# Optimization experiments

Hardware: AMD Instinct MI355X
Metric: run time of the kernel (lower is better)

Reference implementation:

```python
import jax, jax.numpy as jnp
import numpy as np

B = 16384
D_VIS, D_LANG, D_STATE = 768, 768, 64
D = 256          # d_model
E = 4            # n_experts
K = 2            # top_k
D_IN = D_VIS + D_LANG + D_STATE
EPS = 1e-5


def layernorm(x, g, b):
    mu = x.mean(-1, keepdims=True)
    var = ((x - mu) ** 2).mean(-1, keepdims=True)
    return g * (x - mu) / jnp.sqrt(var + EPS) + b


def setup_inputs() -> dict:
    key = jax.random.key(0)
    ks = jax.random.split(key, 16)
    s = 0.02
    return {
        "vis": jax.random.normal(ks[0], (B, D_VIS), jnp.float32),
        "lang": jax.random.normal(ks[1], (B, D_LANG), jnp.float32),
        "state": jax.random.normal(ks[2], (B, D_STATE), jnp.float32),
        # fusion: Linear(d_in, d_model) + LayerNorm
        "Wf": jax.random.normal(ks[3], (D_IN, D), jnp.float32) * s,
        "bf": jnp.zeros((D,), jnp.float32),
        "gf": jnp.ones((D,), jnp.float32),
        "bfln": jnp.zeros((D,), jnp.float32),
        # gate (bias=False); random instead of zeros so routing is nontrivial
        "Wg": jax.random.normal(ks[4], (D, E), jnp.float32) * s,
        # stacked experts: Linear(d,2d) -> GELU -> Linear(2d,d) -> GELU -> Linear(d,d), then LN(x + net(x))
        "W1": jax.random.normal(ks[5], (E, D, 2 * D), jnp.float32) * s,
        "b1": jnp.zeros((E, 2 * D), jnp.float32),
        "W2": jax.random.normal(ks[6], (E, 2 * D, D), jnp.float32) * s,
        "b2": jnp.zeros((E, D), jnp.float32),
        "W3": jax.random.normal(ks[7], (E, D, D), jnp.float32) * s,
        "b3": jnp.zeros((E, D), jnp.float32),
        "eg": jnp.ones((E, D), jnp.float32),
        "eb": jnp.zeros((E, D), jnp.float32),
    }


def reference(vis, lang, state, Wf, bf, gf, bfln, Wg, W1, b1, W2, b2, W3, b3, eg, eb):
    gelu = lambda t: jax.nn.gelu(t, approximate=False)
    # fusion: Linear -> LayerNorm -> GELU  (dropout is eval-mode identity)
    x = jnp.concatenate([vis, lang, state], axis=-1) @ Wf + bf   # [B, D]
    x = gelu(layernorm(x, gf, bfln))

    logits = x @ Wg                                              # [B, E]
    all_probs = jax.nn.softmax(logits, axis=-1)
    top_vals, top_idx = jax.lax.top_k(logits, K)                 # [B, K]
    top_w = jax.nn.softmax(top_vals, axis=-1)                    # [B, K]

    # all experts densely (E small); original computes same math per masked subset
    h = gelu(jnp.einsum('bd,edh->beh', x, W1) + b1)              # [B, E, 2D]
    h = gelu(jnp.einsum('beh,ehd->bed', h, W2) + b2)             # [B, E, D]
    h = jnp.einsum('bed,edf->bef', h, W3) + b3                   # [B, E, D]
    y = layernorm(x[:, None, :] + h, eg, eb)                     # [B, E, D]

    # gather selected experts and combine with top-k weights
    y_sel = jnp.take_along_axis(y, top_idx[:, :, None], axis=1)  # [B, K, D]
    out = jnp.einsum('bk,bkd->bd', top_w, y_sel)                 # [B, D]

    # load-balance loss: importance x load
    counts = jnp.zeros((E,), x.dtype).at[top_idx.reshape(-1)].add(1.0)
    f_i = counts / (B * K)
    lb_loss = E * jnp.sum(f_i * all_probs.mean(0))
    return out, lb_loss
```

## Files before the change

### kernel.cpp

```cpp
#include <hip/hip_runtime.h>
#include <math.h>


typedef unsigned short u16;
typedef unsigned int u32;
typedef __attribute__((ext_vector_type(8))) short bf16x8;
typedef __attribute__((ext_vector_type(4))) float f32x4;

__device__ __forceinline__ float bf2f(u16 u) {
    union { u32 i; float f; } v; v.i = ((u32)u) << 16; return v.f;
}
__device__ __forceinline__ u16 f2bf(float f) {
    union { float f; u32 i; } v; v.f = f;
    u32 x = v.i;
    return (u16)((x + 0x7fffu + ((x >> 16) & 1u)) >> 16);
}
__device__ __forceinline__ float gelu_exact(float v) {
    return 0.5f * v * (1.0f + erff(v * 0.70710678118654752f));
}

typedef __attribute__((address_space(1))) void GV;
typedef __attribute__((address_space(3))) void SV;
__device__ __forceinline__ void gldlds(const void* g, void* l) {
    __builtin_amdgcn_global_load_lds((GV*)g, (SV*)l, 16, 0, 0);
}

__device__ __forceinline__ u32 pk2(u32 f0, u32 f1) {
    return __builtin_amdgcn_perm(f1, f0, 0x07060302);
}

__device__ __forceinline__ void stageA64(const u16* Ag, int lda, u16* As, int tid) {
#pragma unroll
    for (int i = 0; i < 2; ++i) {
        int s = i * 256 + tid;
        int m = s >> 3, c = s & 7;
        gldlds(Ag + m * lda + (c ^ (m & 7)) * 8, As + s * 8);
    }
}
__device__ __forceinline__ void stageA64_R32(const u16* Ag, int lda, u16* As, int tid) {
    int s = tid;
    int m = s >> 3, c = s & 7;
    gldlds(Ag + m * lda + (c ^ (m & 7)) * 8, As + s * 8);
}
__device__ __forceinline__ void stageB64(const u16* Bg, int ldb, u16* Bs, int tid) {
#pragma unroll
    for (int i = 0; i < 8; ++i) {
        int s = i * 256 + tid;
        int n = s >> 3, c = s & 7;
        gldlds(Bg + n * ldb + (c ^ (n & 7)) * 8, Bs + s * 8);
    }
}
__device__ __forceinline__ void compute64(const u16* As, const u16* Bs, f32x4 acc[4][4],
                                          int w, int l16, int quad) {
#pragma unroll
    for (int ks = 0; ks < 2; ++ks) {
        bf16x8 a[4];
#pragma unroll
        for (int mt = 0; mt < 4; ++mt) {
            int m = mt * 16 + l16;
            a[mt] = *(const bf16x8*)(As + m * 64 + (((ks * 4 + quad) ^ (m & 7)) << 3));
        }
#pragma unroll
        for (int nt = 0; nt < 4; ++nt) {
            int n = w * 64 + nt * 16 + l16;
            bf16x8 b = *(const bf16x8*)(Bs + n * 64 + (((ks * 4 + quad) ^ (n & 7)) << 3));
#pragma unroll
            for (int mt = 0; mt < 4; ++mt)
                acc[mt][nt] = __builtin_amdgcn_mfma_f32_16x16x32_bf16(a[mt], b, acc[mt][nt], 0, 0, 0);
        }
    }
}
__device__ __forceinline__ void compute64_R32(const u16* As, const u16* Bs, f32x4 acc[2][4],
                                              int w, int l16, int quad) {
#pragma unroll
    for (int ks = 0; ks < 2; ++ks) {
        bf16x8 a[2];
#pragma unroll
        for (int mt = 0; mt < 2; ++mt) {
            int m = mt * 16 + l16;
            a[mt] = *(const bf16x8*)(As + m * 64 + (((ks * 4 + quad) ^ (m & 7)) << 3));
        }
#pragma unroll
        for (int nt = 0; nt < 4; ++nt) {
            int n = w * 64 + nt * 16 + l16;
            bf16x8 b = *(const bf16x8*)(Bs + n * 64 + (((ks * 4 + quad) ^ (n & 7)) << 3));
#pragma unroll
            for (int mt = 0; mt < 2; ++mt)
                acc[mt][nt] = __builtin_amdgcn_mfma_f32_16x16x32_bf16(a[mt], b, acc[mt][nt], 0, 0, 0);
        }
    }
}

#define SEG_WF  409600
#define SEG_W1  524288
#define SEG_W2  524288
#define SEG_W3  262144
#define PREP_ITEMS (SEG_WF + SEG_W1 + SEG_W2 + SEG_W3 + 8)

__global__ __launch_bounds__(256) void prep_kernel(
    const float* __restrict__ Wf, const float* __restrict__ W1, const float* __restrict__ W2,
    const float* __restrict__ W3,
    u16* __restrict__ wft, u16* __restrict__ w1t, u16* __restrict__ w2t, u16* __restrict__ w3t,
    float* __restrict__ lbacc) {
    int idx = blockIdx.x * 256 + threadIdx.x;
    if (idx < SEG_WF) {
        int n = idx / 1600, k = idx % 1600;
        wft[idx] = f2bf(Wf[(size_t)k * 256 + n]);
        return;
    }
    idx -= SEG_WF;
    if (idx < SEG_W1) {
        int e = idx >> 17, r = idx & 131071;
        int n = r >> 8, k = r & 255;
        w1t[idx] = f2bf(W1[(size_t)e * 131072 + (size_t)k * 512 + n]);
        return;
    }
    idx -= SEG_W1;
    if (idx < SEG_W2) {
        int e = idx >> 17, r = idx & 131071;
        int n = r >> 9, k = r & 511;
        w2t[idx] = f2bf(W2[(size_t)e * 131072 + (size_t)k * 256 + n]);
        return;
    }
    idx -= SEG_W2;
    if (idx < SEG_W3) {
        int e = idx >> 16, r = idx & 65535;
        int n = r >> 8, k = r & 255;
        w3t[idx] = f2bf(W3[(size_t)e * 65536 + (size_t)k * 256 + n]);
        return;
    }
    idx -= SEG_W3;
    if (idx < 8) lbacc[idx] = 0.0f;
}

__global__ __launch_bounds__(256) void fusion_kernel(
    const float* __restrict__ vis, const float* __restrict__ lang, const float* __restrict__ state,
    const u16* __restrict__ BT, const float* __restrict__ bfv_, const float* __restrict__ gf,
    const float* __restrict__ bfln, const float* __restrict__ Wg,
    u16* __restrict__ xbf, float* __restrict__ wr, float* __restrict__ lbacc) {
    __shared__ __align__(16) u32 Af[2048];
    __shared__ __align__(16) u16 Bs[16384];
    int tid = threadIdx.x;
    int w = tid >> 6, lane = tid & 63, quad = lane >> 4, l16 = lane & 15;
    int m0 = blockIdx.x * 32;
    f32x4 acc[2][4] = {};

    for (int kit = 0; kit < 25; ++kit) {
        const float* base; int ld;
        if (kit < 12)      { base = vis   + (size_t)m0 * 768 + kit * 64;        ld = 768; }
        else if (kit < 24) { base = lang  + (size_t)m0 * 768 + (kit - 12) * 64; ld = 768; }
        else               { base = state + (size_t)m0 * 64;                    ld = 64; }
#pragma unroll
        for (int i = 0; i < 2; ++i) {
            int s = i * 256 + tid;
            int m = s >> 4, c = s & 15;
            gldlds(base + m * ld + (c ^ (m & 15)) * 4, Af + s * 4);
        }
        stageB64(BT + kit * 64, 1600, Bs, tid);
        __syncthreads();
#pragma unroll
        for (int ks = 0; ks < 2; ++ks) {
            bf16x8 a[2];
#pragma unroll
            for (int mt = 0; mt < 2; ++mt) {
                int m = mt * 16 + l16;
                int c0 = ks * 8 + quad * 2;
                const u32* rowp = Af + m * 64;
                uint4 f0 = *(const uint4*)(rowp + (c0 ^ (m & 15)) * 4);
                uint4 f1 = *(const uint4*)(rowp + ((c0 + 1) ^ (m & 15)) * 4);
                union { u32 u[4]; bf16x8 v; } pk;
                pk.u[0] = pk2(f0.x, f0.y); pk.u[1] = pk2(f0.z, f0.w);
                pk.u[2] = pk2(f1.x, f1.y); pk.u[3] = pk2(f1.z, f1.w);
                a[mt] = pk.v;
            }
#pragma unroll
            for (int nt = 0; nt < 4; ++nt) {
                int n = w * 64 + nt * 16 + l16;
                bf16x8 b = *(const bf16x8*)(Bs + n * 64 + (((ks * 4 + quad) ^ (n & 7)) << 3));
#pragma unroll
                for (int mt = 0; mt < 2; ++mt)
                    acc[mt][nt] = __builtin_amdgcn_mfma_f32_16x16x32_bf16(a[mt], b, acc[mt][nt], 0, 0, 0);
            }
        }
        __syncthreads();
    }

    float2* red  = (float2*)Af;
    float*  muv  = (float*)(Af + 256);
    float*  rsv  = (float*)(Af + 288);
    float*  gred = (float*)(Af + 512);
    float*  sacc = (float*)(Af + 1024);

    float bv[4], gvv[4], blv[4]; float4 wgv[4];
#pragma unroll
    for (int nt = 0; nt < 4; ++nt) {
        int col = w * 64 + nt * 16 + l16;
        bv[nt] = bfv_[col]; gvv[nt] = gf[col]; blv[nt] = bfln[col];
        wgv[nt] = *(const float4*)(Wg + col * 4);
    }
    if (tid < 8) sacc[tid] = 0.f;
#pragma unroll
    for (int mt = 0; mt < 2; ++mt)
#pragma unroll
        for (int r = 0; r < 4; ++r) {
            float ss = 0.f, qq = 0.f;
#pragma unroll
            for (int nt = 0; nt < 4; ++nt) {
                float v = acc[mt][nt][r] + bv[nt];
                acc[mt][nt][r] = v;
                ss += v; qq += v * v;
            }
#pragma unroll
            for (int d = 1; d < 16; d <<= 1) { ss += __shfl_xor(ss, d); qq += __shfl_xor(qq, d); }
            if (l16 == 0) red[w * 32 + mt * 16 + quad * 4 + r] = make_float2(ss, qq);
        }
    __syncthreads();
    if (tid < 32) {
        float ss = 0.f, qq = 0.f;
#pragma unroll
        for (int ww = 0; ww < 4; ++ww) { float2 t = red[ww * 32 + tid]; ss += t.x; qq += t.y; }
        float mu = ss * (1.f / 256.f);
        float var = qq * (1.f / 256.f) - mu * mu;
        muv[tid] = mu;
        rsv[tid] = 1.f / sqrtf(var + 1e-5f);
    }
    __syncthreads();
#pragma unroll
    for (int mt = 0; mt < 2; ++mt)
#pragma unroll
        for (int r = 0; r < 4; ++r) {
            int rl = mt * 16 + quad * 4 + r;
            float mu = muv[rl], rs = rsv[rl];
#pragma unroll
            for (int nt = 0; nt < 4; ++nt) {
                int col = w * 64 + nt * 16 + l16;
                float t = (acc[mt][nt][r] - mu) * rs * gvv[nt] + blv[nt];
                float g = gelu_exact(t);
                acc[mt][nt][r] = g;
                xbf[(size_t)(m0 + rl) * 256 + col] = f2bf(g);
            }
        }
#pragma unroll
    for (int mt = 0; mt < 2; ++mt)
#pragma unroll
        for (int r = 0; r < 4; ++r) {
            int rl = mt * 16 + quad * 4 + r;
            float p0 = 0.f, p1 = 0.f, p2 = 0.f, p3 = 0.f;
#pragma unroll
            for (int nt = 0; nt < 4; ++nt) {
                float g = acc[mt][nt][r];
                p0 += g * wgv[nt].x; p1 += g * wgv[nt].y;
                p2 += g * wgv[nt].z; p3 += g * wgv[nt].w;
            }
#pragma unroll
            for (int d = 1; d < 16; d <<= 1) {
                p0 += __shfl_xor(p0, d); p1 += __shfl_xor(p1, d);
                p2 += __shfl_xor(p2, d); p3 += __shfl_xor(p3, d);
            }
            if (l16 == 0) {
                float* gp = gred + w * 128 + rl * 4;
                gp[0] = p0; gp[1] = p1; gp[2] = p2; gp[3] = p3;
            }
        }
    __syncthreads();
    if (tid < 32) {
        int row = tid;
        float lg[4];
#pragma unroll
        for (int e = 0; e < 4; ++e)
            lg[e] = gred[row * 4 + e] + gred[128 + row * 4 + e] +
                    gred[256 + row * 4 + e] + gred[384 + row * 4 + e];
        float mx = fmaxf(fmaxf(lg[0], lg[1]), fmaxf(lg[2], lg[3]));
        float ex[4]; float Z = 0.f;
#pragma unroll
        for (int e = 0; e < 4; ++e) { ex[e] = expf(lg[e] - mx); Z += ex[e]; }
        int i0 = 0; float v0 = lg[0];
#pragma unroll
        for (int e = 1; e < 4; ++e) if (lg[e] > v0) { v0 = lg[e]; i0 = e; }
        int i1 = -1; float v1 = -1e30f;
#pragma unroll
        for (int e = 0; e < 4; ++e) if (e != i0 && lg[e] > v1) { v1 = lg[e]; i1 = e; }
        float t = expf(v1 - v0);
        float wA = 1.f / (1.f + t), wB = t / (1.f + t);
        float w4[4] = {0.f, 0.f, 0.f, 0.f};
        w4[i0] = wA; w4[i1] = wB;
#pragma unroll
        for (int e = 0; e < 4; ++e) wr[(size_t)(m0 + row) * 4 + e] = w4[e];
#pragma unroll
        for (int e = 0; e < 4; ++e) atomicAdd(&sacc[e], ex[e] / Z);
        atomicAdd(&sacc[4 + i0], 1.f);
        atomicAdd(&sacc[4 + i1], 1.f);
    }
    __syncthreads();
    if (tid < 8) atomicAdd(lbacc + tid, sacc[tid]);
}

__global__ __launch_bounds__(256) void expert_gemm_kernel(
    const u16* __restrict__ A, int lda, size_t aE,
    const u16* __restrict__ BT, size_t bE,
    const float* __restrict__ bias, int biasE,
    u16* __restrict__ outp, int ldo, size_t oE) {
    __shared__ __align__(16) u16 As[4096];
    __shared__ __align__(16) u16 Bs[16384];
    int tid = threadIdx.x;
    int w = tid >> 6, lane = tid & 63, quad = lane >> 4, l16 = lane & 15;
    int m0 = blockIdx.x * 64;
    int col0 = blockIdx.y * 256;
    int e = blockIdx.z;
    f32x4 acc[4][4] = {};
    const u16* Ag = A + e * aE + (size_t)m0 * lda;
    const u16* Bg = BT + e * bE + (size_t)col0 * lda;
    int kiters = lda >> 6;
    for (int kit = 0; kit < kiters; ++kit) {
        stageA64(Ag + kit * 64, lda, As, tid);
        stageB64(Bg + kit * 64, lda, Bs, tid);
        __syncthreads();
        compute64(As, Bs, acc, w, l16, quad);
        __syncthreads();
    }
#pragma unroll
    for (int nt = 0; nt < 4; ++nt) {
        int col = col0 + w * 64 + nt * 16 + l16;
        float bvv = bias[e * biasE + col];
#pragma unroll
        for (int mt = 0; mt < 4; ++mt)
#pragma unroll
            for (int r = 0; r < 4; ++r) {
                int row = m0 + mt * 16 + quad * 4 + r;
                outp[e * oE + (size_t)row * ldo + col] = f2bf(gelu_exact(acc[mt][nt][r] + bvv));
            }
    }
}

__global__ __launch_bounds__(256) void combine_kernel(
    const u16* __restrict__ h2, const u16* __restrict__ W3T,
    const float* __restrict__ b3, const float* __restrict__ eg, const float* __restrict__ eb,
    const u16* __restrict__ xbf, const float* __restrict__ wr,
    const float* __restrict__ lbacc, float* __restrict__ outp) {
    __shared__ __align__(16) u16 As[2048];
    __shared__ __align__(16) u16 Bs[16384];
    __shared__ __align__(16) u16 xs[8192];
    __shared__ float wl[128];
    int tid = threadIdx.x;
    int w = tid >> 6, lane = tid & 63, quad = lane >> 4, l16 = lane & 15;
    int m0 = blockIdx.x * 32;
    if (blockIdx.x == 0 && tid == 0) {
        float lb = 0.f;
#pragma unroll
        for (int e = 0; e < 4; ++e)
            lb += (lbacc[4 + e] / 32768.f) * (lbacc[e] / 16384.f);
        outp[4194304] = 4.f * lb;
    }
#pragma unroll
    for (int i = 0; i < 4; ++i) {
        int s = i * 256 + tid;
        *(uint4*)(xs + s * 8) = *(const uint4*)(xbf + (size_t)m0 * 256 + s * 8);
    }
    if (tid < 128) wl[tid] = wr[(size_t)m0 * 4 + tid];
    float2* red = (float2*)As;
    float* muv = (float*)((char*)As + 1024);
    float* rsv = (float*)((char*)As + 1152);
    f32x4 oacc[2][4] = {};
    for (int e = 0; e < 4; ++e) {
        __syncthreads();
        f32x4 acc[2][4] = {};
        const u16* Ag = h2 + ((size_t)e * 16384 + m0) * 256;
        const u16* Bg = W3T + (size_t)e * 65536;
        for (int kit = 0; kit < 4; ++kit) {
            stageA64_R32(Ag + kit * 64, 256, As, tid);
            stageB64(Bg + kit * 64, 256, Bs, tid);
            __syncthreads();
            compute64_R32(As, Bs, acc, w, l16, quad);
            __syncthreads();
        }
        float b3v[4], egv[4], ebv[4];
#pragma unroll
        for (int nt = 0; nt < 4; ++nt) {
            int col = w * 64 + nt * 16 + l16;
            b3v[nt] = b3[e * 256 + col]; egv[nt] = eg[e * 256 + col]; ebv[nt] = eb[e * 256 + col];
        }
#pragma unroll
        for (int mt = 0; mt < 2; ++mt)
#pragma unroll
            for (int r = 0; r < 4; ++r) {
                int rl = mt * 16 + quad * 4 + r;
                float ss = 0.f, qq = 0.f;
#pragma unroll
                for (int nt = 0; nt < 4; ++nt) {
                    int col = w * 64 + nt * 16 + l16;
                    float v = acc[mt][nt][r] + b3v[nt] + bf2f(xs[rl * 256 + col]);
                    acc[mt][nt][r] = v;
                    ss += v; qq += v * v;
                }
#pragma unroll
                for (int d = 1; d < 16; d <<= 1) { ss += __shfl_xor(ss, d); qq += __shfl_xor(qq, d); }
                if (l16 == 0) red[w * 32 + rl] = make_float2(ss, qq);
            }
        __syncthreads();
        if (tid < 32) {
            float ss = 0.f, qq = 0.f;
#pragma unroll
            for (int ww = 0; ww < 4; ++ww) { float2 t = red[ww * 32 + tid]; ss += t.x; qq += t.y; }
            float mu = ss * (1.f / 256.f);
            float var = qq * (1.f / 256.f) - mu * mu;
            muv[tid] = mu;
            rsv[tid] = 1.f / sqrtf(var + 1e-5f);
        }
        __syncthreads();
#pragma unroll
        for (int mt = 0; mt < 2; ++mt)
#pragma unroll
            for (int r = 0; r < 4; ++r) {
                int rl = mt * 16 + quad * 4 + r;
                float mu = muv[rl], rs = rsv[rl], we = wl[rl * 4 + e];
#pragma unroll
                for (int nt = 0; nt < 4; ++nt) {
                    float y = (acc[mt][nt][r] - mu) * rs * egv[nt] + ebv[nt];
                    oacc[mt][nt][r] += we * y;
                }
            }
    }
#pragma unroll
    for (int mt = 0; mt < 2; ++mt)
#pragma unroll
        for (int r = 0; r < 4; ++r) {
            int rl = mt * 16 + quad * 4 + r;
#pragma unroll
            for (int nt = 0; nt < 4; ++nt) {
                int col = w * 64 + nt * 16 + l16;
                outp[(size_t)(m0 + rl) * 256 + col] = oacc[mt][nt][r];
            }
        }
}

extern "C" void kernel_launch(void* const* d_in, const int* in_sizes, int n_in,
                              void* d_out, int out_size, void* d_ws, size_t ws_size,
                              hipStream_t stream) {
    const float* vis   = (const float*)d_in[0];
    const float* lang  = (const float*)d_in[1];
    const float* state = (const float*)d_in[2];
    const float* Wf    = (const float*)d_in[3];
    const float* bf_   = (const float*)d_in[4];
    const float* gf    = (const float*)d_in[5];
    const float* bfln  = (const float*)d_in[6];
    const float* Wg    = (const float*)d_in[7];
    const float* W1    = (const float*)d_in[8];
    const float* b1    = (const float*)d_in[9];
    const float* W2    = (const float*)d_in[10];
    const float* b2    = (const float*)d_in[11];
    const float* W3    = (const float*)d_in[12];
    const float* b3    = (const float*)d_in[13];
    const float* eg    = (const float*)d_in[14];
    const float* eb    = (const float*)d_in[15];
    float* outp = (float*)d_out;

    char* ws = (char*)d_ws;
    size_t off = 0;
    float* lbacc = (float*)(ws + off); off += 256;
    u16* WFT  = (u16*)(ws + off); off += 819200UL;
    u16* W1T  = (u16*)(ws + off); off += 1048576UL;
    u16* W2T  = (u16*)(ws + off); off += 1048576UL;
    u16* W3T  = (u16*)(ws + off); off += 524288UL;
    u16* XBF  = (u16*)(ws + off); off += 8388608UL;
    float* WR = (float*)(ws + off); off += 262144UL;
    u16* H1   = (u16*)(ws + off); off += 67108864UL;
    u16* H2   = (u16*)(ws + off); off += 33554432UL;
    if (ws_size < off) return;

    int prep_blocks = (PREP_ITEMS + 255) / 256;
    prep_kernel<<<prep_blocks, 256, 0, stream>>>(Wf, W1, W2, W3, WFT, W1T, W2T, W3T, lbacc);
    fusion_kernel<<<512, 256, 0, stream>>>(vis, lang, state, WFT, bf_, gf, bfln, Wg,
                                           XBF, WR, lbacc);
    expert_gemm_kernel<<<dim3(256, 2, 4), 256, 0, stream>>>(
        XBF, 256, 0, W1T, 131072, b1, 512, H1, 512, 8388608UL);
    expert_gemm_kernel<<<dim3(256, 1, 4), 256, 0, stream>>>(
        H1, 512, 8388608UL, W2T, 131072, b2, 256, H2, 256, 4194304UL);
    combine_kernel<<<512, 256, 0, stream>>>(H2, W3T, b3, eg, eb, XBF, WR, lbacc, outp);
}
```

Before: 322.4 us.

## Double-buffer GEMM staging, retile expert GEMMs, use fast GELU approximation

Adds double-buffered LDS staging to the fusion, expert and combine kernels so global loads for the next K-slice overlap the MFMA work on the current one. Expert GEMMs now use 64x128 tiles with twice as many blocks. The combine kernel keeps the H2 fragments and the residual x in registers and flattens the expert/k loop into one pipelined loop. Exact erf GELU is replaced with a sigmoid-based tanh approximation, which is cheaper but slightly changes numerics.

```diff
diff --git a/kernel.cpp b/kernel.cpp
--- a/kernel.cpp
+++ b/kernel.cpp
@@ -15,80 +15,18 @@
     u32 x = v.i;
     return (u16)((x + 0x7fffu + ((x >> 16) & 1u)) >> 16);
 }
-__device__ __forceinline__ float gelu_exact(float v) {
-    return 0.5f * v * (1.0f + erff(v * 0.70710678118654752f));
+__device__ __forceinline__ float gelu_fast(float x) {
+    float t = x * (1.59576912f + 0.07135481f * x * x);
+    return x / (1.f + __expf(-t));
+}
+__device__ __forceinline__ u32 pk2(u32 f0, u32 f1) {
+    return __builtin_amdgcn_perm(f1, f0, 0x07060302);
 }
 
 typedef __attribute__((address_space(1))) void GV;
 typedef __attribute__((address_space(3))) void SV;
 __device__ __forceinline__ void gldlds(const void* g, void* l) {
     __builtin_amdgcn_global_load_lds((GV*)g, (SV*)l, 16, 0, 0);
-}
-
-__device__ __forceinline__ u32 pk2(u32 f0, u32 f1) {
-    return __builtin_amdgcn_perm(f1, f0, 0x07060302);
-}
-
-__device__ __forceinline__ void stageA64(const u16* Ag, int lda, u16* As, int tid) {
-#pragma unroll
-    for (int i = 0; i < 2; ++i) {
-        int s = i * 256 + tid;
-        int m = s >> 3, c = s & 7;
-        gldlds(Ag + m * lda + (c ^ (m & 7)) * 8, As + s * 8);
-    }
-}
-__device__ __forceinline__ void stageA64_R32(const u16* Ag, int lda, u16* As, int tid) {
-    int s = tid;
-    int m = s >> 3, c = s & 7;
-    gldlds(Ag + m * lda + (c ^ (m & 7)) * 8, As + s * 8);
-}
-__device__ __forceinline__ void stageB64(const u16* Bg, int ldb, u16* Bs, int tid) {
-#pragma unroll
-    for (int i = 0; i < 8; ++i) {
-        int s = i * 256 + tid;
-        int n = s >> 3, c = s & 7;
-        gldlds(Bg + n * ldb + (c ^ (n & 7)) * 8, Bs + s * 8);
-    }
-}
-__device__ __forceinline__ void compute64(const u16* As, const u16* Bs, f32x4 acc[4][4],
-                                          int w, int l16, int quad) {
-#pragma unroll
-    for (int ks = 0; ks < 2; ++ks) {
-        bf16x8 a[4];
-#pragma unroll
-        for (int mt = 0; mt < 4; ++mt) {
-            int m = mt * 16 + l16;
-            a[mt] = *(const bf16x8*)(As + m * 64 + (((ks * 4 + quad) ^ (m & 7)) << 3));
-        }
-#pragma unroll
-        for (int nt = 0; nt < 4; ++nt) {
-            int n = w * 64 + nt * 16 + l16;
-            bf16x8 b = *(const bf16x8*)(Bs + n * 64 + (((ks * 4 + quad) ^ (n & 7)) << 3));
-#pragma unroll
-            for (int mt = 0; mt < 4; ++mt)
-                acc[mt][nt] = __builtin_amdgcn_mfma_f32_16x16x32_bf16(a[mt], b, acc[mt][nt], 0, 0, 0);
-        }
-    }
-}
-__device__ __forceinline__ void compute64_R32(const u16* As, const u16* Bs, f32x4 acc[2][4],
-                                              int w, int l16, int quad) {
-#pragma unroll
-    for (int ks = 0; ks < 2; ++ks) {
-        bf16x8 a[2];
-#pragma unroll
-        for (int mt = 0; mt < 2; ++mt) {
-            int m = mt * 16 + l16;
-            a[mt] = *(const bf16x8*)(As + m * 64 + (((ks * 4 + quad) ^ (m & 7)) << 3));
-        }
-#pragma unroll
-        for (int nt = 0; nt < 4; ++nt) {
-            int n = w * 64 + nt * 16 + l16;
-            bf16x8 b = *(const bf16x8*)(Bs + n * 64 + (((ks * 4 + quad) ^ (n & 7)) << 3));
-#pragma unroll
-            for (int mt = 0; mt < 2; ++mt)
-                acc[mt][nt] = __builtin_amdgcn_mfma_f32_16x16x32_bf16(a[mt], b, acc[mt][nt], 0, 0, 0);
-        }
-    }
 }
 
 #define SEG_WF  409600
@@ -138,58 +76,68 @@
     const u16* __restrict__ BT, const float* __restrict__ bfv_, const float* __restrict__ gf,
     const float* __restrict__ bfln, const float* __restrict__ Wg,
     u16* __restrict__ xbf, float* __restrict__ wr, float* __restrict__ lbacc) {
-    __shared__ __align__(16) u32 Af[2048];
-    __shared__ __align__(16) u16 Bs[16384];
-    int tid = threadIdx.x;
-    int w = tid >> 6, lane = tid & 63, quad = lane >> 4, l16 = lane & 15;
+    __shared__ __align__(16) u32 Af[2][2048];
+    __shared__ __align__(16) u16 Bs[2][16384];
+    int tid = threadIdx.x, w = tid >> 6, lane = tid & 63, quad = lane >> 4, l16 = lane & 15;
     int m0 = blockIdx.x * 32;
     f32x4 acc[2][4] = {};
 
-    for (int kit = 0; kit < 25; ++kit) {
+    auto stageAB = [&](int kit, int buf) {
         const float* base; int ld;
-        if (kit < 12)      { base = vis   + (size_t)m0 * 768 + kit * 64;        ld = 768; }
-        else if (kit < 24) { base = lang  + (size_t)m0 * 768 + (kit - 12) * 64; ld = 768; }
-        else               { base = state + (size_t)m0 * 64;                    ld = 64; }
+        if (kit < 12)      { base = vis + kit * 64;          ld = 768; }
+        else if (kit < 24) { base = lang + (kit - 12) * 64;  ld = 768; }
+        else               { base = state;                   ld = 64; }
+        base += (size_t)m0 * ld;
 #pragma unroll
         for (int i = 0; i < 2; ++i) {
-            int s = i * 256 + tid;
-            int m = s >> 4, c = s & 15;
-            gldlds(base + m * ld + (c ^ (m & 15)) * 4, Af + s * 4);
-        }
-        stageB64(BT + kit * 64, 1600, Bs, tid);
-        __syncthreads();
+            int s = i * 256 + tid, m = s >> 4, c = s & 15;
+            gldlds(base + (size_t)m * ld + ((c ^ (m & 15)) << 2), &Af[buf][s * 4]);
+        }
+#pragma unroll
+        for (int i = 0; i < 8; ++i) {
+            int s = i * 256 + tid, n = s >> 3, c = s & 7;
+            gldlds(BT + (size_t)n * 1600 + kit * 64 + ((c ^ (n & 7)) << 3), &Bs[buf][s * 8]);
+        }
+    };
+    auto comp = [&](int buf) {
 #pragma unroll
         for (int ks = 0; ks < 2; ++ks) {
-            bf16x8 a[2];
+            bf16x8 av[2];
 #pragma unroll
             for (int mt = 0; mt < 2; ++mt) {
                 int m = mt * 16 + l16;
                 int c0 = ks * 8 + quad * 2;
-                const u32* rowp = Af + m * 64;
-                uint4 f0 = *(const uint4*)(rowp + (c0 ^ (m & 15)) * 4);
-                uint4 f1 = *(const uint4*)(rowp + ((c0 + 1) ^ (m & 15)) * 4);
+                const u32* rowp = &Af[buf][m * 64];
+                uint4 f0 = *(const uint4*)(rowp + ((c0 ^ (m & 15)) << 2));
+                uint4 f1 = *(const uint4*)(rowp + (((c0 + 1) ^ (m & 15)) << 2));
                 union { u32 u[4]; bf16x8 v; } pk;
                 pk.u[0] = pk2(f0.x, f0.y); pk.u[1] = pk2(f0.z, f0.w);
                 pk.u[2] = pk2(f1.x, f1.y); pk.u[3] = pk2(f1.z, f1.w);
-                a[mt] = pk.v;
+                av[mt] = pk.v;
             }
 #pragma unroll
             for (int nt = 0; nt < 4; ++nt) {
                 int n = w * 64 + nt * 16 + l16;
-                bf16x8 b = *(const bf16x8*)(Bs + n * 64 + (((ks * 4 + quad) ^ (n & 7)) << 3));
+                bf16x8 b = *(const bf16x8*)(&Bs[buf][n * 64 + (((ks * 4 + quad) ^ (n & 7)) << 3)]);
 #pragma unroll
                 for (int mt = 0; mt < 2; ++mt)
-                    acc[mt][nt] = __builtin_amdgcn_mfma_f32_16x16x32_bf16(a[mt], b, acc[mt][nt], 0, 0, 0);
-            }
-        }
+                    acc[mt][nt] = __builtin_amdgcn_mfma_f32_16x16x32_bf16(av[mt], b, acc[mt][nt], 0, 0, 0);
+            }
+        }
+    };
+
+    stageAB(0, 0);
+    for (int k = 0; k < 25; ++k) {
         __syncthreads();
-    }
-
-    float2* red  = (float2*)Af;
-    float*  muv  = (float*)(Af + 256);
-    float*  rsv  = (float*)(Af + 288);
-    float*  gred = (float*)(Af + 512);
-    float*  sacc = (float*)(Af + 1024);
+        if (k < 24) stageAB(k + 1, (k + 1) & 1);
+        comp(k & 1);
+    }
+    u32* SC = (u32*)(&Bs[1][0]);
+    float2* red  = (float2*)SC;
+    float*  muv  = (float*)(SC + 256);
+    float*  rsv  = (float*)(SC + 288);
+    float*  gred = (float*)(SC + 512);
+    float*  sacc = (float*)(SC + 1024);
 
     float bv[4], gvv[4], blv[4]; float4 wgv[4];
 #pragma unroll
@@ -235,7 +183,7 @@
             for (int nt = 0; nt < 4; ++nt) {
                 int col = w * 64 + nt * 16 + l16;
                 float t = (acc[mt][nt][r] - mu) * rs * gvv[nt] + blv[nt];
-                float g = gelu_exact(t);
+                float g = gelu_fast(t);
                 acc[mt][nt][r] = g;
                 xbf[(size_t)(m0 + rl) * 256 + col] = f2bf(g);
             }
@@ -295,39 +243,71 @@
     if (tid < 8) atomicAdd(lbacc + tid, sacc[tid]);
 }
 
-__global__ __launch_bounds__(256) void expert_gemm_kernel(
-    const u16* __restrict__ A, int lda, size_t aE,
-    const u16* __restrict__ BT, size_t bE,
+template<int KITS>
+__global__ __launch_bounds__(256) void expert_kernel(
+    const u16* __restrict__ A, int lda, long aE,
+    const u16* __restrict__ BT, long bE,
     const float* __restrict__ bias, int biasE,
-    u16* __restrict__ outp, int ldo, size_t oE) {
-    __shared__ __align__(16) u16 As[4096];
-    __shared__ __align__(16) u16 Bs[16384];
-    int tid = threadIdx.x;
-    int w = tid >> 6, lane = tid & 63, quad = lane >> 4, l16 = lane & 15;
+    u16* __restrict__ outp, int ldo, long oE) {
+    __shared__ __align__(16) u16 As[2][4096];
+    __shared__ __align__(16) u16 Bs[2][8192];
+    int tid = threadIdx.x, w = tid >> 6, lane = tid & 63, quad = lane >> 4, l16 = lane & 15;
     int m0 = blockIdx.x * 64;
-    int col0 = blockIdx.y * 256;
+    int n0 = blockIdx.y * 128;
     int e = blockIdx.z;
-    f32x4 acc[4][4] = {};
-    const u16* Ag = A + e * aE + (size_t)m0 * lda;
-    const u16* Bg = BT + e * bE + (size_t)col0 * lda;
-    int kiters = lda >> 6;
-    for (int kit = 0; kit < kiters; ++kit) {
-        stageA64(Ag + kit * 64, lda, As, tid);
-        stageB64(Bg + kit * 64, lda, Bs, tid);
+    const u16* Ag = A + (size_t)e * aE + (size_t)m0 * lda;
+    const u16* Bg = BT + (size_t)e * bE + (size_t)n0 * lda;
+    f32x4 acc[4][2] = {};
+
+    auto stage = [&](int kit, int buf) {
+#pragma unroll
+        for (int i = 0; i < 2; ++i) {
+            int s = i * 256 + tid, m = s >> 3, c = s & 7;
+            gldlds(Ag + (size_t)m * lda + kit * 64 + ((c ^ (m & 7)) << 3), &As[buf][s * 8]);
+        }
+#pragma unroll
+        for (int i = 0; i < 4; ++i) {
+            int s = i * 256 + tid, n = s >> 3, c = s & 7;
+            gldlds(Bg + (size_t)n * lda + kit * 64 + ((c ^ (n & 7)) << 3), &Bs[buf][s * 8]);
+        }
+    };
+    auto comp = [&](int buf) {
+#pragma unroll
+        for (int ks = 0; ks < 2; ++ks) {
+            bf16x8 av[4];
+#pragma unroll
+            for (int mt = 0; mt < 4; ++mt) {
+                int m = mt * 16 + l16;
+                av[mt] = *(const bf16x8*)(&As[buf][m * 64 + (((ks * 4 + quad) ^ (m & 7)) << 3)]);
+            }
+#pragma unroll
+            for (int nt = 0; nt < 2; ++nt) {
+                int n = w * 32 + nt * 16 + l16;
+                bf16x8 b = *(const bf16x8*)(&Bs[buf][n * 64 + (((ks * 4 + quad) ^ (n & 7)) << 3)]);
+#pragma unroll
+                for (int mt = 0; mt < 4; ++mt)
+                    acc[mt][nt] = __builtin_amdgcn_mfma_f32_16x16x32_bf16(av[mt], b, acc[mt][nt], 0, 0, 0);
+            }
+        }
+    };
+
+    stage(0, 0);
+    for (int k = 0; k < KITS; ++k) {
         __syncthreads();
-        compute64(As, Bs, acc, w, l16, quad);
-        __syncthreads();
-    }
-#pragma unroll
-    for (int nt = 0; nt < 4; ++nt) {
-        int col = col0 + w * 64 + nt * 16 + l16;
+        if (k + 1 < KITS) stage(k + 1, (k + 1) & 1);
+        comp(k & 1);
+    }
+
+#pragma unroll
+    for (int nt = 0; nt < 2; ++nt) {
+        int col = n0 + w * 32 + nt * 16 + l16;
         float bvv = bias[e * biasE + col];
 #pragma unroll
         for (int mt = 0; mt < 4; ++mt)
 #pragma unroll
             for (int r = 0; r < 4; ++r) {
                 int row = m0 + mt * 16 + quad * 4 + r;
-                outp[e * oE + (size_t)row * ldo + col] = f2bf(gelu_exact(acc[mt][nt][r] + bvv));
+                outp[(size_t)e * oE + (size_t)row * ldo + col] = f2bf(gelu_fast(acc[mt][nt][r] + bvv));
             }
     }
 }
@@ -337,12 +317,11 @@
     const float* __restrict__ b3, const float* __restrict__ eg, const float* __restrict__ eb,
     const u16* __restrict__ xbf, const float* __restrict__ wr,
     const float* __restrict__ lbacc, float* __restrict__ outp) {
-    __shared__ __align__(16) u16 As[2048];
-    __shared__ __align__(16) u16 Bs[16384];
-    __shared__ __align__(16) u16 xs[8192];
+    __shared__ __align__(16) u16 Bs[2][16384];
     __shared__ float wl[128];
-    int tid = threadIdx.x;
-    int w = tid >> 6, lane = tid & 63, quad = lane >> 4, l16 = lane & 15;
+    __shared__ float2 red[128];
+    __shared__ float muv[32], rsv[32];
+    int tid = threadIdx.x, w = tid >> 6, lane = tid & 63, quad = lane >> 4, l16 = lane & 15;
     int m0 = blockIdx.x * 32;
     if (blockIdx.x == 0 && tid == 0) {
         float lb = 0.f;
@@ -351,74 +330,109 @@
             lb += (lbacc[4 + e] / 32768.f) * (lbacc[e] / 16384.f);
         outp[4194304] = 4.f * lb;
     }
-#pragma unroll
-    for (int i = 0; i < 4; ++i) {
-        int s = i * 256 + tid;
-        *(uint4*)(xs + s * 8) = *(const uint4*)(xbf + (size_t)m0 * 256 + s * 8);
-    }
+    u16 xr[2][2][4];
+    u16 xrr[2][4][4];
+#pragma unroll
+    for (int mt = 0; mt < 2; ++mt)
+#pragma unroll
+        for (int r = 0; r < 4; ++r) {
+            int row = m0 + mt * 16 + quad * 4 + r;
+#pragma unroll
+            for (int nt = 0; nt < 4; ++nt)
+                xrr[mt][nt][r] = xbf[(size_t)row * 256 + w * 64 + nt * 16 + l16];
+        }
+    (void)xr;
     if (tid < 128) wl[tid] = wr[(size_t)m0 * 4 + tid];
-    float2* red = (float2*)As;
-    float* muv = (float*)((char*)As + 1024);
-    float* rsv = (float*)((char*)As + 1152);
+
+    auto stageB = [&](int u, int buf) {
+        int e = u >> 2, kit = u & 3;
+        const u16* Bg = W3T + (size_t)e * 65536;
+#pragma unroll
+        for (int i = 0; i < 8; ++i) {
+            int s = i * 256 + tid, n = s >> 3, c = s & 7;
+            gldlds(Bg + (size_t)n * 256 + kit * 64 + ((c ^ (n & 7)) << 3), &Bs[buf][s * 8]);
+        }
+    };
+    uint4 aR[2][2][2];
+    auto loadA = [&](int u, int ring) {
+        int e = u >> 2, kit = u & 3;
+#pragma unroll
+        for (int mt = 0; mt < 2; ++mt) {
+            const u16* p = h2 + ((size_t)e * 16384 + m0 + mt * 16 + l16) * 256 + kit * 64 + quad * 8;
+            aR[ring][mt][0] = *(const uint4*)p;
+            aR[ring][mt][1] = *(const uint4*)(p + 16);
+        }
+    };
+
     f32x4 oacc[2][4] = {};
-    for (int e = 0; e < 4; ++e) {
+    f32x4 acc[2][4] = {};
+    stageB(0, 0); loadA(0, 0);
+#pragma unroll 4
+    for (int u = 0; u < 16; ++u) {
         __syncthreads();
-        f32x4 acc[2][4] = {};
-        const u16* Ag = h2 + ((size_t)e * 16384 + m0) * 256;
-        const u16* Bg = W3T + (size_t)e * 65536;
-        for (int kit = 0; kit < 4; ++kit) {
-            stageA64_R32(Ag + kit * 64, 256, As, tid);
-            stageB64(Bg + kit * 64, 256, Bs, tid);
+        if (u < 15) { stageB(u + 1, (u + 1) & 1); loadA(u + 1, (u + 1) & 1); }
+#pragma unroll
+        for (int ks = 0; ks < 2; ++ks) {
+#pragma unroll
+            for (int nt = 0; nt < 4; ++nt) {
+                int n = w * 64 + nt * 16 + l16;
+                bf16x8 b = *(const bf16x8*)(&Bs[u & 1][n * 64 + (((ks * 4 + quad) ^ (n & 7)) << 3)]);
+#pragma unroll
+                for (int mt = 0; mt < 2; ++mt) {
+                    union { uint4 u4; bf16x8 v; } av; av.u4 = aR[u & 1][mt][ks];
+                    acc[mt][nt] = __builtin_amdgcn_mfma_f32_16x16x32_bf16(av.v, b, acc[mt][nt], 0, 0, 0);
+                }
+            }
+        }
+        if ((u & 3) == 3) {
+            int e = u >> 2;
+            float b3v[4], egv[4], ebv[4];
+#pragma unroll
+            for (int nt = 0; nt < 4; ++nt) {
+                int col = w * 64 + nt * 16 + l16;
+                b3v[nt] = b3[e * 256 + col]; egv[nt] = eg[e * 256 + col]; ebv[nt] = eb[e * 256 + col];
+            }
+#pragma unroll
+            for (int mt = 0; mt < 2; ++mt)
+#pragma unroll
+                for (int r = 0; r < 4; ++r) {
+                    int rl = mt * 16 + quad * 4 + r;
+                    float ss = 0.f, qq = 0.f;
+#pragma unroll
+                    for (int nt = 0; nt < 4; ++nt) {
+                        float v = acc[mt][nt][r] + b3v[nt] + bf2f(xrr[mt][nt][r]);
+                        acc[mt][nt][r] = v;
+                        ss += v; qq += v * v;
+                    }
+#pragma unroll
+                    for (int d = 1; d < 16; d <<= 1) { ss += __shfl_xor(ss, d); qq += __shfl_xor(qq, d); }
+                    if (l16 == 0) red[w * 32 + rl] = make_float2(ss, qq);
+                }
             __syncthreads();
-            compute64_R32(As, Bs, acc, w, l16, quad);
+            if (tid < 32) {
+                float ss = 0.f, qq = 0.f;
+#pragma unroll
+                for (int ww = 0; ww < 4; ++ww) { float2 t = red[ww * 32 + tid]; ss += t.x; qq += t.y; }
+                float mu = ss * (1.f / 256.f);
+                float var = qq * (1.f / 256.f) - mu * mu;
+                muv[tid] = mu;
+                rsv[tid] = 1.f / sqrtf(var + 1e-5f);
+            }
             __syncthreads();
-        }
-        float b3v[4], egv[4], ebv[4];
-#pragma unroll
-        for (int nt = 0; nt < 4; ++nt) {
-            int col = w * 64 + nt * 16 + l16;
-            b3v[nt] = b3[e * 256 + col]; egv[nt] = eg[e * 256 + col]; ebv[nt] = eb[e * 256 + col];
-        }
-#pragma unroll
-        for (int mt = 0; mt < 2; ++mt)
-#pragma unroll
-            for (int r = 0; r < 4; ++r) {
-                int rl = mt * 16 + quad * 4 + r;
-                float ss = 0.f, qq = 0.f;
-#pragma unroll
-                for (int nt = 0; nt < 4; ++nt) {
-                    int col = w * 64 + nt * 16 + l16;
-                    float v = acc[mt][nt][r] + b3v[nt] + bf2f(xs[rl * 256 + col]);
-                    acc[mt][nt][r] = v;
-                    ss += v; qq += v * v;
+#pragma unroll
+            for (int mt = 0; mt < 2; ++mt)
+#pragma unroll
+                for (int r = 0; r < 4; ++r) {
+                    int rl = mt * 16 + quad * 4 + r;
+                    float mu = muv[rl], rs = rsv[rl], we = wl[rl * 4 + e];
+#pragma unroll
+                    for (int nt = 0; nt < 4; ++nt) {
+                        float y = (acc[mt][nt][r] - mu) * rs * egv[nt] + ebv[nt];
+                        oacc[mt][nt][r] += we * y;
+                        acc[mt][nt][r] = 0.f;
+                    }
                 }
-#pragma unroll
-                for (int d = 1; d < 16; d <<= 1) { ss += __shfl_xor(ss, d); qq += __shfl_xor(qq, d); }
-                if (l16 == 0) red[w * 32 + rl] = make_float2(ss, qq);
-            }
-        __syncthreads();
-        if (tid < 32) {
-            float ss = 0.f, qq = 0.f;
-#pragma unroll
-            for (int ww = 0; ww < 4; ++ww) { float2 t = red[ww * 32 + tid]; ss += t.x; qq += t.y; }
-            float mu = ss * (1.f / 256.f);
-            float var = qq * (1.f / 256.f) - mu * mu;
-            muv[tid] = mu;
-            rsv[tid] = 1.f / sqrtf(var + 1e-5f);
-        }
-        __syncthreads();
-#pragma unroll
-        for (int mt = 0; mt < 2; ++mt)
-#pragma unroll
-            for (int r = 0; r < 4; ++r) {
-                int rl = mt * 16 + quad * 4 + r;
-                float mu = muv[rl], rs = rsv[rl], we = wl[rl * 4 + e];
-#pragma unroll
-                for (int nt = 0; nt < 4; ++nt) {
-                    float y = (acc[mt][nt][r] - mu) * rs * egv[nt] + ebv[nt];
-                    oacc[mt][nt][r] += we * y;
-                }
-            }
+        }
     }
 #pragma unroll
     for (int mt = 0; mt < 2; ++mt)
@@ -471,9 +485,9 @@
     prep_kernel<<<prep_blocks, 256, 0, stream>>>(Wf, W1, W2, W3, WFT, W1T, W2T, W3T, lbacc);
     fusion_kernel<<<512, 256, 0, stream>>>(vis, lang, state, WFT, bf_, gf, bfln, Wg,
                                            XBF, WR, lbacc);
-    expert_gemm_kernel<<<dim3(256, 2, 4), 256, 0, stream>>>(
-        XBF, 256, 0, W1T, 131072, b1, 512, H1, 512, 8388608UL);
-    expert_gemm_kernel<<<dim3(256, 1, 4), 256, 0, stream>>>(
-        H1, 512, 8388608UL, W2T, 131072, b2, 256, H2, 256, 4194304UL);
+    expert_kernel<4><<<dim3(256, 4, 4), 256, 0, stream>>>(
+        XBF, 256, 0L, W1T, 131072L, b1, 512, H1, 512, 8388608L);
+    expert_kernel<8><<<dim3(256, 2, 4), 256, 0, stream>>>(
+        H1, 512, 8388608L, W2T, 131072L, b2, 256, H2, 256, 4194304L);
     combine_kernel<<<512, 256, 0, stream>>>(H2, W3T, b3, eg, eb, XBF, WR, lbacc, outp);
 }
```

Measured after the change: 342.6 us. +6.3%, slower.
